# Performance work log

Hardware: AMD Instinct MI355X
Metric: run time of the kernel (lower is better)

## Reference

```python
import jax, jax.numpy as jnp
import numpy as np

N = 6144      # nodes
NFEAT = 512
NHID = 256
NHEADS = 4
DHEAD = NHID // NHEADS  # 64
NEMBED = 128
NEG_INF = -9e15
LRELU_ALPHA = 0.2


def setup_inputs() -> dict:
    key = jax.random.key(0)
    k = jax.random.split(key, 8)
    x = jax.random.normal(k[0], (N, NFEAT), dtype=jnp.float32)
    adj = (jax.random.uniform(k[1], (N, N)) < 0.01).astype(jnp.int32)
    # per-head GAT params, packed over heads
    W = jax.random.normal(k[2], (NHEADS, NFEAT, DHEAD), dtype=jnp.float32) * 0.05
    a_src = jax.random.normal(k[3], (NHEADS, DHEAD), dtype=jnp.float32) * 0.05
    a_dst = jax.random.normal(k[4], (NHEADS, DHEAD), dtype=jnp.float32) * 0.05
    # output linear (init.normal_ std=0.05 per reset_parameters)
    lin_w = jax.random.normal(k[5], (NEMBED, NHID), dtype=jnp.float32) * 0.05
    lin_b = jnp.zeros((NEMBED,), dtype=jnp.float32)
    return {"x": x, "adj": adj, "W": W, "a_src": a_src, "a_dst": a_dst,
            "lin_w": lin_w, "lin_b": lin_b}


def _gat_forward(x, adj, W, a_src, a_dst, lin_w, lin_b):
    # Wh: [H, N, D]
    Wh = jnp.einsum('nf,hfd->hnd', x, W)
    # attention logits e_ij = leakyrelu(a_src.Wh_i + a_dst.Wh_j): [H, N, N]
    s = jnp.einsum('hnd,hd->hn', Wh, a_src)   # source term per node
    t = jnp.einsum('hnd,hd->hn', Wh, a_dst)   # target term per node
    e = s[:, :, None] + t[:, None, :]
    e = jax.nn.leaky_relu(e, negative_slope=LRELU_ALPHA)
    # mask by adjacency, softmax over neighbors
    e = jnp.where(adj[None, :, :] > 0, e, NEG_INF)
    attn = jax.nn.softmax(e, axis=-1)
    # aggregate and per-head ELU (concat=True GAT layer)
    h = jnp.einsum('hnm,hmd->hnd', attn, Wh)
    h = jax.nn.elu(h)
    # concat heads -> [N, NHID]
    h = jnp.transpose(h, (1, 0, 2)).reshape(N, NHID)
    # dropout is identity in eval mode; linear + ELU
    out = jax.nn.elu(h @ lin_w.T + lin_b)
    return out


def reference(x, adj, W, a_src, a_dst, lin_w, lin_b):
    return _gat_forward(x, adj, W, a_src, a_dst, lin_w, lin_b)
```

## Files before the change

### kernel.cpp

```cpp
#include <hip/hip_runtime.h>
#include <hip/hip_bf16.h>
#include <math.h>

#define N_NODES 6144
#define NFEAT 512
#define NHID 256
#define NHEADS 4
#define DHEAD 64
#define NEMBED 128
#define LRELU_ALPHA 0.2f
#define MAXC 256

__global__ __launch_bounds__(256) void wh_gemm(const float* __restrict__ x,
                                               const float* __restrict__ W,
                                               const float* __restrict__ a_src,
                                               const float* __restrict__ a_dst,
                                               float* __restrict__ Wh,
                                               float* __restrict__ s_arr,
                                               float* __restrict__ t_arr) {
    __shared__ float As[64][16];
    __shared__ float Bs[16][64];
    const int tid = threadIdx.x;
    const int tx = tid & 15;
    const int ty = tid >> 4;
    const int row0 = blockIdx.x * 64;
    const int h = blockIdx.y;
    const float* Bp = W + (size_t)h * NFEAT * DHEAD;

    float acc[4][4] = {};

    for (int k0 = 0; k0 < NFEAT; k0 += 16) {
        {
            const int r = tid >> 2, kq = tid & 3;
            const float4 v = *(const float4*)(x + (size_t)(row0 + r) * NFEAT + k0 + kq * 4);
            *(float4*)&As[r][kq * 4] = v;
        }
        {
            const int kk = tid >> 4, cq = tid & 15;
            const float4 v = *(const float4*)(Bp + (size_t)(k0 + kk) * DHEAD + cq * 4);
            *(float4*)&Bs[kk][cq * 4] = v;
        }
        __syncthreads();
#pragma unroll
        for (int kk = 0; kk < 16; kk++) {
            float a[4], b[4];
#pragma unroll
            for (int i = 0; i < 4; i++) a[i] = As[ty * 4 + i][kk];
#pragma unroll
            for (int j = 0; j < 4; j++) b[j] = Bs[kk][tx * 4 + j];
#pragma unroll
            for (int i = 0; i < 4; i++)
#pragma unroll
                for (int j = 0; j < 4; j++) acc[i][j] += a[i] * b[j];
        }
        __syncthreads();
    }
#pragma unroll
    for (int i = 0; i < 4; i++) {
        const int row = row0 + ty * 4 + i;
        float4 v = make_float4(acc[i][0], acc[i][1], acc[i][2], acc[i][3]);
        *(float4*)(Wh + ((size_t)h * N_NODES + row) * DHEAD + tx * 4) = v;
    }
    float a4s[4], a4d[4];
#pragma unroll
    for (int j = 0; j < 4; j++) {
        a4s[j] = a_src[h * DHEAD + tx * 4 + j];
        a4d[j] = a_dst[h * DHEAD + tx * 4 + j];
    }
#pragma unroll
    for (int i = 0; i < 4; i++) {
        float ps = acc[i][0] * a4s[0] + acc[i][1] * a4s[1] +
                   acc[i][2] * a4s[2] + acc[i][3] * a4s[3];
        float pt = acc[i][0] * a4d[0] + acc[i][1] * a4d[1] +
                   acc[i][2] * a4d[2] + acc[i][3] * a4d[3];
#pragma unroll
        for (int off = 1; off < 16; off <<= 1) {
            ps += __shfl_xor(ps, off);
            pt += __shfl_xor(pt, off);
        }
        if (tx == 0) {
            const int row = row0 + ty * 4 + i;
            s_arr[h * N_NODES + row] = ps;
            t_arr[h * N_NODES + row] = pt;
        }
    }
}

__global__ __launch_bounds__(256) void attn_agg(const int* __restrict__ adj,
                                                const float* __restrict__ Wh,
                                                const float* __restrict__ s_arr,
                                                const float* __restrict__ t_arr,
                                                float* __restrict__ hcat) {
    __shared__ unsigned short nbr[N_NODES];
    __shared__ float p_s[NHEADS][MAXC];
    __shared__ int cnt;
    const int i = blockIdx.x;
    const int tid = threadIdx.x;
    const int wid = tid >> 6;
    const int lane = tid & 63;
    if (tid == 0) cnt = 0;
    __syncthreads();

    const int* arow = adj + (size_t)i * N_NODES;
    const unsigned long long lower = (1ull << lane) - 1ull;
#pragma unroll
    for (int it = 0; it < 6; ++it) {
        const int j0 = it * 1024 + wid * 256 + lane * 4;
        const int4 v = *(const int4*)(arow + j0);
        const unsigned long long b0 = __ballot(v.x != 0);
        const unsigned long long b1 = __ballot(v.y != 0);
        const unsigned long long b2 = __ballot(v.z != 0);
        const unsigned long long b3 = __ballot(v.w != 0);
        const int n0 = __popcll(b0), n1 = __popcll(b1);
        const int n2 = __popcll(b2), n3 = __popcll(b3);
        const int tot = n0 + n1 + n2 + n3;
        int base = 0;
        if (lane == 0 && tot) base = atomicAdd(&cnt, tot);
        base = __shfl(base, 0);
        if (v.x) nbr[base + __popcll(b0 & lower)] = (unsigned short)j0;
        base += n0;
        if (v.y) nbr[base + __popcll(b1 & lower)] = (unsigned short)(j0 + 1);
        base += n1;
        if (v.z) nbr[base + __popcll(b2 & lower)] = (unsigned short)(j0 + 2);
        base += n2;
        if (v.w) nbr[base + __popcll(b3 & lower)] = (unsigned short)(j0 + 3);
    }
    __syncthreads();
    const int c = cnt;

    const int h = wid;
    const float s_h = s_arr[h * N_NODES + i];
    const float* tp = t_arr + (size_t)h * N_NODES;
    const float* whp = Wh + (size_t)h * N_NODES * DHEAD;

    float acc, l;
    if (c > 0 && c <= MAXC) {
        float m = -INFINITY;
        for (int k = lane; k < c; k += 64) {
            float e = s_h + tp[nbr[k]];
            e = e >= 0.0f ? e : LRELU_ALPHA * e;
            p_s[h][k] = e;
            m = fmaxf(m, e);
        }
#pragma unroll
        for (int off = 32; off > 0; off >>= 1) m = fmaxf(m, __shfl_xor(m, off));
        float ls = 0.0f;
        for (int k = lane; k < c; k += 64) {
            const float p = __expf(p_s[h][k] - m);
            p_s[h][k] = p;
            ls += p;
        }
#pragma unroll
        for (int off = 32; off > 0; off >>= 1) ls += __shfl_xor(ls, off);
        l = ls;

        float a0 = 0.f, a1 = 0.f, a2 = 0.f, a3 = 0.f;
        float a4 = 0.f, a5 = 0.f, a6 = 0.f, a7 = 0.f;
        int k = 0;
        for (; k + 8 <= c; k += 8) {
            const int j0 = nbr[k],     j1 = nbr[k + 1], j2 = nbr[k + 2], j3 = nbr[k + 3];
            const int j4 = nbr[k + 4], j5 = nbr[k + 5], j6 = nbr[k + 6], j7 = nbr[k + 7];
            const float p0 = p_s[h][k],     p1 = p_s[h][k + 1];
            const float p2 = p_s[h][k + 2], p3 = p_s[h][k + 3];
            const float p4 = p_s[h][k + 4], p5 = p_s[h][k + 5];
            const float p6 = p_s[h][k + 6], p7 = p_s[h][k + 7];
            a0 += p0 * whp[(size_t)j0 * DHEAD + lane];
            a1 += p1 * whp[(size_t)j1 * DHEAD + lane];
            a2 += p2 * whp[(size_t)j2 * DHEAD + lane];
            a3 += p3 * whp[(size_t)j3 * DHEAD + lane];
            a4 += p4 * whp[(size_t)j4 * DHEAD + lane];
            a5 += p5 * whp[(size_t)j5 * DHEAD + lane];
            a6 += p6 * whp[(size_t)j6 * DHEAD + lane];
            a7 += p7 * whp[(size_t)j7 * DHEAD + lane];
        }
        for (; k < c; k++) a0 += p_s[h][k] * whp[(size_t)nbr[k] * DHEAD + lane];
        acc = ((a0 + a1) + (a2 + a3)) + ((a4 + a5) + (a6 + a7));
    } else if (c == 0) {
        acc = 0.0f;
        for (int j = 0; j < N_NODES; j++) acc += whp[(size_t)j * DHEAD + lane];
        l = (float)N_NODES;
    } else {
        float m = -INFINITY, ll = 0.0f;
        acc = 0.0f;
        for (int k = 0; k < c; k++) {
            const int j = nbr[k];
            float e = s_h + tp[j];
            e = e >= 0.0f ? e : LRELU_ALPHA * e;
            const float m_new = fmaxf(m, e);
            const float scale = __expf(m - m_new);
            const float p = __expf(e - m_new);
            ll = ll * scale + p;
            acc = acc * scale + p * whp[(size_t)j * DHEAD + lane];
            m = m_new;
        }
        l = ll;
    }
    float hv = acc / l;
    hv = hv > 0.0f ? hv : expm1f(hv);
    hcat[(size_t)i * NHID + h * DHEAD + lane] = hv;
}

__global__ __launch_bounds__(256) void out_gemm(const float* __restrict__ hcat,
                                                const float* __restrict__ lin_w,
                                                const float* __restrict__ lin_b,
                                                float* __restrict__ out) {
    __shared__ float As[64][16];
    __shared__ float Bs[16][64];
    const int tid = threadIdx.x;
    const int tx = tid & 15;
    const int ty = tid >> 4;
    const int row0 = blockIdx.x * 64;
    const int c0 = blockIdx.y * 64;

    float acc[4][4] = {};

    for (int k0 = 0; k0 < NHID; k0 += 16) {
        {
            const int r = tid >> 2, kq = tid & 3;
            const float4 v = *(const float4*)(hcat + (size_t)(row0 + r) * NHID + k0 + kq * 4);
            *(float4*)&As[r][kq * 4] = v;
        }
        {
            const int cc = tid & 63, kq = tid >> 6;
            const float4 v = *(const float4*)(lin_w + (size_t)(c0 + cc) * NHID + k0 + kq * 4);
            Bs[kq * 4 + 0][cc] = v.x;
            Bs[kq * 4 + 1][cc] = v.y;
            Bs[kq * 4 + 2][cc] = v.z;
            Bs[kq * 4 + 3][cc] = v.w;
        }
        __syncthreads();
#pragma unroll
        for (int kk = 0; kk < 16; kk++) {
            float a[4], b[4];
#pragma unroll
            for (int i = 0; i < 4; i++) a[i] = As[ty * 4 + i][kk];
#pragma unroll
            for (int j = 0; j < 4; j++) b[j] = Bs[kk][tx * 4 + j];
#pragma unroll
            for (int i = 0; i < 4; i++)
#pragma unroll
                for (int j = 0; j < 4; j++) acc[i][j] += a[i] * b[j];
        }
        __syncthreads();
    }
#pragma unroll
    for (int i = 0; i < 4; i++) {
        const int row = row0 + ty * 4 + i;
        float v[4];
#pragma unroll
        for (int j = 0; j < 4; j++) {
            const int col = c0 + tx * 4 + j;
            float val = acc[i][j] + lin_b[col];
            v[j] = val > 0.0f ? val : expm1f(val);
        }
        *(float4*)(out + (size_t)row * NEMBED + c0 + tx * 4) =
            make_float4(v[0], v[1], v[2], v[3]);
    }
}

extern "C" void kernel_launch(void* const* d_in, const int* in_sizes, int n_in,
                              void* d_out, int out_size, void* d_ws, size_t ws_size,
                              hipStream_t stream) {
    const float* x     = (const float*)d_in[0];
    const int*   adj   = (const int*)d_in[1];
    const float* W     = (const float*)d_in[2];
    const float* a_src = (const float*)d_in[3];
    const float* a_dst = (const float*)d_in[4];
    const float* lin_w = (const float*)d_in[5];
    const float* lin_b = (const float*)d_in[6];
    float* out = (float*)d_out;

    float* Wh   = (float*)d_ws;
    float* s    = Wh + (size_t)NHEADS * N_NODES * DHEAD;
    float* t    = s + (size_t)NHEADS * N_NODES;
    float* hcat = t + (size_t)NHEADS * N_NODES;

    wh_gemm<<<dim3(N_NODES / 64, NHEADS), 256, 0, stream>>>(x, W, a_src, a_dst, Wh, s, t);
    attn_agg<<<N_NODES, 256, 0, stream>>>(adj, Wh, s, t, hcat);
    out_gemm<<<dim3(N_NODES / 64, NEMBED / 64), 256, 0, stream>>>(hcat, lin_w, lin_b, out);
}
```

Before: 308.0 us.

## Move adjacency scan into GEMM kernel as extra blocks to overlap with Wh GEMM

```diff
diff --git a/kernel.cpp b/kernel.cpp
--- a/kernel.cpp
+++ b/kernel.cpp
@@ -10,78 +10,130 @@
 #define NEMBED 128
 #define LRELU_ALPHA 0.2f
 #define MAXC 256
-
-__global__ __launch_bounds__(256) void wh_gemm(const float* __restrict__ x,
-                                               const float* __restrict__ W,
-                                               const float* __restrict__ a_src,
-                                               const float* __restrict__ a_dst,
-                                               float* __restrict__ Wh,
-                                               float* __restrict__ s_arr,
-                                               float* __restrict__ t_arr) {
-    __shared__ float As[64][16];
-    __shared__ float Bs[16][64];
+#define SCAN_BLOCKS 384
+#define ROWS_PER_SCAN 16
+
+__global__ __launch_bounds__(256) void gemm_scan(const float* __restrict__ x,
+                                                 const float* __restrict__ W,
+                                                 const float* __restrict__ a_src,
+                                                 const float* __restrict__ a_dst,
+                                                 const int* __restrict__ adj,
+                                                 float* __restrict__ Wh,
+                                                 float* __restrict__ s_arr,
+                                                 float* __restrict__ t_arr,
+                                                 int* __restrict__ cnt_g,
+                                                 unsigned short* __restrict__ nbr_g) {
+    __shared__ union SM {
+        struct { float As[64][16]; float Bs[16][64]; } g;
+        struct { unsigned short nbr[MAXC]; int cnt; } s;
+    } sm;
     const int tid = threadIdx.x;
-    const int tx = tid & 15;
-    const int ty = tid >> 4;
-    const int row0 = blockIdx.x * 64;
-    const int h = blockIdx.y;
-    const float* Bp = W + (size_t)h * NFEAT * DHEAD;
-
-    float acc[4][4] = {};
-
-    for (int k0 = 0; k0 < NFEAT; k0 += 16) {
-        {
-            const int r = tid >> 2, kq = tid & 3;
-            const float4 v = *(const float4*)(x + (size_t)(row0 + r) * NFEAT + k0 + kq * 4);
-            *(float4*)&As[r][kq * 4] = v;
-        }
-        {
-            const int kk = tid >> 4, cq = tid & 15;
-            const float4 v = *(const float4*)(Bp + (size_t)(k0 + kk) * DHEAD + cq * 4);
-            *(float4*)&Bs[kk][cq * 4] = v;
-        }
-        __syncthreads();
-#pragma unroll
-        for (int kk = 0; kk < 16; kk++) {
-            float a[4], b[4];
-#pragma unroll
-            for (int i = 0; i < 4; i++) a[i] = As[ty * 4 + i][kk];
-#pragma unroll
-            for (int j = 0; j < 4; j++) b[j] = Bs[kk][tx * 4 + j];
-#pragma unroll
-            for (int i = 0; i < 4; i++)
-#pragma unroll
-                for (int j = 0; j < 4; j++) acc[i][j] += a[i] * b[j];
-        }
-        __syncthreads();
-    }
-#pragma unroll
-    for (int i = 0; i < 4; i++) {
-        const int row = row0 + ty * 4 + i;
-        float4 v = make_float4(acc[i][0], acc[i][1], acc[i][2], acc[i][3]);
-        *(float4*)(Wh + ((size_t)h * N_NODES + row) * DHEAD + tx * 4) = v;
-    }
-    float a4s[4], a4d[4];
-#pragma unroll
-    for (int j = 0; j < 4; j++) {
-        a4s[j] = a_src[h * DHEAD + tx * 4 + j];
-        a4d[j] = a_dst[h * DHEAD + tx * 4 + j];
-    }
-#pragma unroll
-    for (int i = 0; i < 4; i++) {
-        float ps = acc[i][0] * a4s[0] + acc[i][1] * a4s[1] +
-                   acc[i][2] * a4s[2] + acc[i][3] * a4s[3];
-        float pt = acc[i][0] * a4d[0] + acc[i][1] * a4d[1] +
-                   acc[i][2] * a4d[2] + acc[i][3] * a4d[3];
-#pragma unroll
-        for (int off = 1; off < 16; off <<= 1) {
-            ps += __shfl_xor(ps, off);
-            pt += __shfl_xor(pt, off);
-        }
-        if (tx == 0) {
+
+    if (blockIdx.y < NHEADS) {
+        const int tx = tid & 15;
+        const int ty = tid >> 4;
+        const int row0 = blockIdx.x * 64;
+        const int h = blockIdx.y;
+        const float* Bp = W + (size_t)h * NFEAT * DHEAD;
+
+        float acc[4][4] = {};
+
+        for (int k0 = 0; k0 < NFEAT; k0 += 16) {
+            {
+                const int r = tid >> 2, kq = tid & 3;
+                const float4 v = *(const float4*)(x + (size_t)(row0 + r) * NFEAT + k0 + kq * 4);
+                *(float4*)&sm.g.As[r][kq * 4] = v;
+            }
+            {
+                const int kk = tid >> 4, cq = tid & 15;
+                const float4 v = *(const float4*)(Bp + (size_t)(k0 + kk) * DHEAD + cq * 4);
+                *(float4*)&sm.g.Bs[kk][cq * 4] = v;
+            }
+            __syncthreads();
+#pragma unroll
+            for (int kk = 0; kk < 16; kk++) {
+                float a[4], b[4];
+#pragma unroll
+                for (int i = 0; i < 4; i++) a[i] = sm.g.As[ty * 4 + i][kk];
+#pragma unroll
+                for (int j = 0; j < 4; j++) b[j] = sm.g.Bs[kk][tx * 4 + j];
+#pragma unroll
+                for (int i = 0; i < 4; i++)
+#pragma unroll
+                    for (int j = 0; j < 4; j++) acc[i][j] += a[i] * b[j];
+            }
+            __syncthreads();
+        }
+#pragma unroll
+        for (int i = 0; i < 4; i++) {
             const int row = row0 + ty * 4 + i;
-            s_arr[h * N_NODES + row] = ps;
-            t_arr[h * N_NODES + row] = pt;
+            float4 v = make_float4(acc[i][0], acc[i][1], acc[i][2], acc[i][3]);
+            *(float4*)(Wh + ((size_t)h * N_NODES + row) * DHEAD + tx * 4) = v;
+        }
+        float a4s[4], a4d[4];
+#pragma unroll
+        for (int j = 0; j < 4; j++) {
+            a4s[j] = a_src[h * DHEAD + tx * 4 + j];
+            a4d[j] = a_dst[h * DHEAD + tx * 4 + j];
+        }
+#pragma unroll
+        for (int i = 0; i < 4; i++) {
+            float ps = acc[i][0] * a4s[0] + acc[i][1] * a4s[1] +
+                       acc[i][2] * a4s[2] + acc[i][3] * a4s[3];
+            float pt = acc[i][0] * a4d[0] + acc[i][1] * a4d[1] +
+                       acc[i][2] * a4d[2] + acc[i][3] * a4d[3];
+#pragma unroll
+            for (int off = 1; off < 16; off <<= 1) {
+                ps += __shfl_xor(ps, off);
+                pt += __shfl_xor(pt, off);
+            }
+            if (tx == 0) {
+                const int row = row0 + ty * 4 + i;
+                s_arr[h * N_NODES + row] = ps;
+                t_arr[h * N_NODES + row] = pt;
+            }
+        }
+    } else {
+        const int scan_id = (blockIdx.y - NHEADS) * gridDim.x + blockIdx.x;
+        const int wid = tid >> 6;
+        const int lane = tid & 63;
+        const unsigned long long lower = (1ull << lane) - 1ull;
+
+        for (int q = 0; q < ROWS_PER_SCAN; ++q) {
+            const int r = scan_id + q * SCAN_BLOCKS;
+            if (tid == 0) sm.s.cnt = 0;
+            __syncthreads();
+            const int* arow = adj + (size_t)r * N_NODES;
+#pragma unroll
+            for (int it = 0; it < 6; ++it) {
+                const int j0 = it * 1024 + wid * 256 + lane * 4;
+                const int4 v = *(const int4*)(arow + j0);
+                const unsigned long long b0 = __ballot(v.x != 0);
+                const unsigned long long b1 = __ballot(v.y != 0);
+                const unsigned long long b2 = __ballot(v.z != 0);
+                const unsigned long long b3 = __ballot(v.w != 0);
+                const int n0 = __popcll(b0), n1 = __popcll(b1);
+                const int n2 = __popcll(b2), n3 = __popcll(b3);
+                const int tot = n0 + n1 + n2 + n3;
+                int base = 0;
+                if (lane == 0 && tot) base = atomicAdd(&sm.s.cnt, tot);
+                base = __shfl(base, 0);
+                int p;
+                if (v.x) { p = base + __popcll(b0 & lower); if (p < MAXC) sm.s.nbr[p] = (unsigned short)j0; }
+                base += n0;
+                if (v.y) { p = base + __popcll(b1 & lower); if (p < MAXC) sm.s.nbr[p] = (unsigned short)(j0 + 1); }
+                base += n1;
+                if (v.z) { p = base + __popcll(b2 & lower); if (p < MAXC) sm.s.nbr[p] = (unsigned short)(j0 + 2); }
+                base += n2;
+                if (v.w) { p = base + __popcll(b3 & lower); if (p < MAXC) sm.s.nbr[p] = (unsigned short)(j0 + 3); }
+            }
+            __syncthreads();
+            const int c = sm.s.cnt;
+            const int cc = c < MAXC ? c : MAXC;
+            for (int k = tid; k < cc; k += 256)
+                nbr_g[(size_t)r * MAXC + k] = sm.s.nbr[k];
+            if (tid == 0) cnt_g[r] = c;
+            __syncthreads();
         }
     }
 }
@@ -90,51 +142,25 @@
                                                 const float* __restrict__ Wh,
                                                 const float* __restrict__ s_arr,
                                                 const float* __restrict__ t_arr,
+                                                const int* __restrict__ cnt_g,
+                                                const unsigned short* __restrict__ nbr_g,
                                                 float* __restrict__ hcat) {
-    __shared__ unsigned short nbr[N_NODES];
+    __shared__ unsigned short nbr[MAXC];
     __shared__ float p_s[NHEADS][MAXC];
-    __shared__ int cnt;
     const int i = blockIdx.x;
     const int tid = threadIdx.x;
-    const int wid = tid >> 6;
+    const int h = tid >> 6;
     const int lane = tid & 63;
-    if (tid == 0) cnt = 0;
-    __syncthreads();
-
-    const int* arow = adj + (size_t)i * N_NODES;
-    const unsigned long long lower = (1ull << lane) - 1ull;
-#pragma unroll
-    for (int it = 0; it < 6; ++it) {
-        const int j0 = it * 1024 + wid * 256 + lane * 4;
-        const int4 v = *(const int4*)(arow + j0);
-        const unsigned long long b0 = __ballot(v.x != 0);
-        const unsigned long long b1 = __ballot(v.y != 0);
-        const unsigned long long b2 = __ballot(v.z != 0);
-        const unsigned long long b3 = __ballot(v.w != 0);
-        const int n0 = __popcll(b0), n1 = __popcll(b1);
-        const int n2 = __popcll(b2), n3 = __popcll(b3);
-        const int tot = n0 + n1 + n2 + n3;
-        int base = 0;
-        if (lane == 0 && tot) base = atomicAdd(&cnt, tot);
-        base = __shfl(base, 0);
-        if (v.x) nbr[base + __popcll(b0 & lower)] = (unsigned short)j0;
-        base += n0;
-        if (v.y) nbr[base + __popcll(b1 & lower)] = (unsigned short)(j0 + 1);
-        base += n1;
-        if (v.z) nbr[base + __popcll(b2 & lower)] = (unsigned short)(j0 + 2);
-        base += n2;
-        if (v.w) nbr[base + __popcll(b3 & lower)] = (unsigned short)(j0 + 3);
-    }
-    __syncthreads();
-    const int c = cnt;
-
-    const int h = wid;
-    const float s_h = s_arr[h * N_NODES + i];
-    const float* tp = t_arr + (size_t)h * N_NODES;
+    const int c = cnt_g[i];
     const float* whp = Wh + (size_t)h * N_NODES * DHEAD;
 
     float acc, l;
     if (c > 0 && c <= MAXC) {
+        for (int k = tid; k < c; k += 256) nbr[k] = nbr_g[(size_t)i * MAXC + k];
+        __syncthreads();
+
+        const float s_h = s_arr[h * N_NODES + i];
+        const float* tp = t_arr + (size_t)h * N_NODES;
         float m = -INFINITY;
         for (int k = lane; k < c; k += 64) {
             float e = s_h + tp[nbr[k]];
@@ -180,18 +206,22 @@
         for (int j = 0; j < N_NODES; j++) acc += whp[(size_t)j * DHEAD + lane];
         l = (float)N_NODES;
     } else {
+        const int* arow = adj + (size_t)i * N_NODES;
+        const float s_h = s_arr[h * N_NODES + i];
+        const float* tp = t_arr + (size_t)h * N_NODES;
         float m = -INFINITY, ll = 0.0f;
         acc = 0.0f;
-        for (int k = 0; k < c; k++) {
-            const int j = nbr[k];
-            float e = s_h + tp[j];
-            e = e >= 0.0f ? e : LRELU_ALPHA * e;
-            const float m_new = fmaxf(m, e);
-            const float scale = __expf(m - m_new);
-            const float p = __expf(e - m_new);
-            ll = ll * scale + p;
-            acc = acc * scale + p * whp[(size_t)j * DHEAD + lane];
-            m = m_new;
+        for (int j = 0; j < N_NODES; j++) {
+            if (arow[j]) {
+                float e = s_h + tp[j];
+                e = e >= 0.0f ? e : LRELU_ALPHA * e;
+                const float m_new = fmaxf(m, e);
+                const float scale = __expf(m - m_new);
+                const float p = __expf(e - m_new);
+                ll = ll * scale + p;
+                acc = acc * scale + p * whp[(size_t)j * DHEAD + lane];
+                m = m_new;
+            }
         }
         l = ll;
     }
@@ -274,8 +304,11 @@
     float* s    = Wh + (size_t)NHEADS * N_NODES * DHEAD;
     float* t    = s + (size_t)NHEADS * N_NODES;
     float* hcat = t + (size_t)NHEADS * N_NODES;
-
-    wh_gemm<<<dim3(N_NODES / 64, NHEADS), 256, 0, stream>>>(x, W, a_src, a_dst, Wh, s, t);
-    attn_agg<<<N_NODES, 256, 0, stream>>>(adj, Wh, s, t, hcat);
+    int* cnt_g  = (int*)(hcat + (size_t)N_NODES * NHID);
+    unsigned short* nbr_g = (unsigned short*)(cnt_g + N_NODES);
+
+    gemm_scan<<<dim3(N_NODES / 64, NHEADS + 4), 256, 0, stream>>>(
+        x, W, a_src, a_dst, adj, Wh, s, t, cnt_g, nbr_g);
+    attn_agg<<<N_NODES, 256, 0, stream>>>(adj, Wh, s, t, cnt_g, nbr_g, hcat);
     out_gemm<<<dim3(N_NODES / 64, NEMBED / 64), 256, 0, stream>>>(hcat, lin_w, lin_b, out);
 }
```

After: 337.7 us. 9.6% more time.
